# Optimization experiments

Hardware: AMD Instinct MI355X
Metric: run time of the kernel (lower is better)

## Reference

```python
import jax, jax.numpy as jnp
import numpy as np

GRID_SPACING = 0.5  # tf.constant(0.5)


def _mlp(x, W1, b1, W2, b2, W3, b3):
    # tiny base_model: 3 -> H -> H -> 1, positive output (softplus head)
    h = jnp.tanh(x @ W1 + b1)
    h = jnp.tanh(h @ W2 + b2)
    return jax.nn.softplus(h @ W3 + b3)


def setup_inputs() -> dict:
    key = jax.random.key(0)
    ks = jax.random.split(key, 8)
    nx = ny = nz = 128
    N = nx * ny * nz
    Ns = (nx - 1) * (ny - 1) * (nz - 1)
    B, H = 32768, 128
    DATAX = jax.random.uniform(ks[0], (N, 3), dtype=jnp.float32)
    DATAF = jax.random.uniform(ks[1], (N, 1), dtype=jnp.float32)
    STAGX = jax.random.uniform(ks[2], (Ns, 3), dtype=jnp.float32)
    LAPLF = jax.random.uniform(ks[3], (nx - 2, ny - 2, nz - 2), dtype=jnp.float32)
    center_indices = jax.random.randint(ks[4], (B,), 0, N, dtype=jnp.int32)
    W1 = jax.random.normal(ks[5], (3, H), dtype=jnp.float32) * 0.5
    W2 = jax.random.normal(ks[6], (H, H), dtype=jnp.float32) * (1.0 / np.sqrt(H))
    W3 = jax.random.normal(ks[7], (H, 1), dtype=jnp.float32) * (1.0 / np.sqrt(H))
    return {
        'DATAX': DATAX, 'DATAF': DATAF, 'STAGX': STAGX, 'LAPLF': LAPLF,
        'loss_m_weight': jnp.full((1,), 0.5, dtype=jnp.float32),
        'W1': W1, 'b1': jnp.zeros((H,), jnp.float32),
        'W2': W2, 'b2': jnp.zeros((H,), jnp.float32),
        'W3': W3, 'b3': jnp.zeros((1,), jnp.float32),
        'center_indices': center_indices,
    }


def reference(DATAX, DATAF, STAGX, LAPLF, loss_m_weight,
              W1, b1, W2, b2, W3, b3, center_indices):
    nxm2, nym2, nzm2 = LAPLF.shape
    nx, ny, nz = nxm2 + 2, nym2 + 2, nzm2 + 2
    N = nx * ny * nz
    Ns = (nx - 1) * (ny - 1) * (nz - 1)
    ci = center_indices.astype(jnp.int32)

    # decode flat id (z-major: z*nx*ny + y*nx + x)
    i_z = ci // (nx * ny)
    rem = ci % (nx * ny)
    i_y = rem // nx
    i_x = rem % nx
    valid = ((i_x >= 1) & (i_x < nx - 1) & (i_y >= 1) & (i_y < ny - 1)
             & (i_z >= 1) & (i_z < nz - 1))

    # 8 original-grid corners: dx,dy,dz in {-1,1}, dz fastest (list-comp order)
    off = jnp.array([-1, 1], jnp.int32)
    dd = jnp.stack(jnp.meshgrid(off, off, off, indexing='ij'), -1).reshape(8, 3)
    ox = i_x[:, None] + dd[None, :, 0]
    oy = i_y[:, None] + dd[None, :, 1]
    oz = i_z[:, None] + dd[None, :, 2]
    flat_o = jnp.clip(oz * nx * ny + oy * nx + ox, 0, N - 1)  # [B,8]

    # 8 staggered-grid corners: dx,dy,dz in {-1,0}, flat = x*ny'*nz' + y*nz' + z
    offs = jnp.array([-1, 0], jnp.int32)
    ds = jnp.stack(jnp.meshgrid(offs, offs, offs, indexing='ij'), -1).reshape(8, 3)
    sx = i_x[:, None] + ds[None, :, 0]
    sy = i_y[:, None] + ds[None, :, 1]
    sz = i_z[:, None] + ds[None, :, 2]
    flat_s = jnp.clip(sx * (ny - 1) * (nz - 1) + sy * (nz - 1) + sz, 0, Ns - 1)

    fo = _mlp(DATAX[flat_o], W1, b1, W2, b2, W3, b3)[..., 0]  # [B,8]
    fs = _mlp(STAGX[flat_s], W1, b1, W2, b2, W3, b3)[..., 0]  # [B,8]

    # diagonals of the [2,2,2] cube: (000,111),(010,101),(001,110),(011,100)
    ia = jnp.array([0, 2, 1, 3])
    ib = jnp.array([7, 5, 6, 4])
    num = jnp.abs(fo[:, ia] + fo[:, ib] - fs[:, ia] - fs[:, ib])
    den = fo[:, ia] + fo[:, ib] + fs[:, ia] + fs[:, ib]
    delta = 3.0 * (GRID_SPACING ** 2)
    lap = jnp.sum(num / den, axis=1) / (3.0 * delta)  # [B]

    flat_l = jnp.clip((i_x - 1) * nym2 * nzm2 + (i_y - 1) * nzm2 + (i_z - 1),
                      0, nxm2 * nym2 * nzm2 - 1)
    dlap = LAPLF.reshape(-1)[flat_l] - lap
    m = valid.astype(dlap.dtype)
    loss_m = loss_m_weight[0] * (jnp.sum(jnp.square(dlap) * m)
                                 / jnp.maximum(jnp.sum(m), 1.0))

    pred = _mlp(DATAX[ci], W1, b1, W2, b2, W3, b3)[:, 0]
    loss_e = jnp.mean(jnp.abs(pred - DATAF[ci][:, 0]))
    return loss_e + loss_m
```

## Files before the change

### kernel.cpp

```cpp
#include <hip/hip_runtime.h>
#include <stdint.h>

#define NXC   128
#define NXY   16384
#define NTOT  2097152
#define NS    2048383
#define SXY   16129
#define SYC   127
#define LXY   15876
#define LTOT  2000376

#define SCALE 2.8853900817779268f

typedef __bf16 bf16x8 __attribute__((ext_vector_type(8)));
typedef float f32x4 __attribute__((ext_vector_type(4)));
typedef float f32x2 __attribute__((ext_vector_type(2)));

typedef const __attribute__((address_space(1))) uint32_t* gas_t;
typedef __attribute__((address_space(3))) uint32_t* las_t;

__device__ __forceinline__ float rcp_hw(float x) {
#if __has_builtin(__builtin_amdgcn_rcpf)
  return __builtin_amdgcn_rcpf(x);
#else
  return 1.0f / x;
#endif
}
__device__ __forceinline__ float exp2_hw(float x) {
#if __has_builtin(__builtin_amdgcn_exp2f)
  return __builtin_amdgcn_exp2f(x);
#else
  return __exp2f(x);
#endif
}

__device__ __forceinline__ f32x2 tanh_pre2(f32x2 z) {
  f32x2 e;
  e.x = exp2_hw(z.x);
  e.y = exp2_hw(z.y);
  f32x2 ep1 = e + 1.0f;
  f32x2 r;
  r.x = rcp_hw(ep1.x);
  r.y = rcp_hw(ep1.y);
  return 1.0f - 2.0f * r;
}
__device__ __forceinline__ float tanh_pre(float z) {
  float e = exp2_hw(z);
  return fmaf(-2.0f, rcp_hw(e + 1.0f), 1.0f);
}

__device__ __forceinline__ float softplus_f(float x) {
  float a = fabsf(x);
  return fmaxf(x, 0.0f) + __logf(1.0f + __expf(-a));
}

__device__ __forceinline__ void ld8v(const float* p, f32x2* o) {
  float4 a = *reinterpret_cast<const float4*>(p);
  float4 b = *reinterpret_cast<const float4*>(p + 4);
  o[0].x = a.x; o[0].y = a.y;
  o[1].x = a.z; o[1].y = a.w;
  o[2].x = b.x; o[2].y = b.y;
  o[3].x = b.z; o[3].y = b.w;
}

__global__ __launch_bounds__(256) void conv_kernel(
    const float* __restrict__ W1, const float* __restrict__ B1,
    const float* __restrict__ W2, const float* __restrict__ B2,
    const float* __restrict__ W3,
    __bf16* __restrict__ w2pre, float* __restrict__ smallpre)
{
  const int n = blockIdx.x * 256 + threadIdx.x;
  if (n < 2048) {
    const int c = n >> 7, j = n & 127;
    bf16x8 v;
    #pragma unroll
    for (int e = 0; e < 8; ++e) v[e] = (__bf16)(SCALE * W2[(8 * c + e) * 128 + j]);
    *reinterpret_cast<bf16x8*>(&w2pre[(j << 7) + (((c ^ (j & 15)) & 15) << 3)]) = v;
  }
  if (blockIdx.x == 0) {
    for (int i = threadIdx.x; i < 768; i += 256) {
      float v;
      if (i < 384)      v = SCALE * W1[i];
      else if (i < 512) v = SCALE * B1[i - 384];
      else if (i < 640) v = SCALE * B2[i - 512];
      else              v = W3[i - 640];
      smallpre[i] = v;
    }
  }
}

__global__ __launch_bounds__(512) void mlp_kernel(
    const float* __restrict__ DATAX, const float* __restrict__ STAGX,
    const int* __restrict__ CI,
    const __bf16* __restrict__ w2pre, const float* __restrict__ smallpre,
    const float* __restrict__ B3, float* __restrict__ fout)
{
  __shared__ __align__(16) __bf16 w2t[16384];
  __shared__ __align__(16) float smallb[768];

  const int tid  = threadIdx.x;
  const int lane = tid & 63;
  const int wid  = tid >> 6;
  const int cl   = lane & 15;
  const int g    = lane >> 4;

  const int group = (blockIdx.x << 3) + wid;
  const int gbase = group << 6;
  const int p = gbase + lane;
  const unsigned bb = (unsigned)p / 17u;
  const int t = p - (int)bb * 17;
  const int ci = CI[bb];

  {
    const char* gsrc = (const char*)w2pre + (wid << 12) + (lane << 4);
    char*       ldst = (char*)w2t + (wid << 12);
    #pragma unroll
    for (int i = 0; i < 4; ++i) {
      __builtin_amdgcn_global_load_lds(
          (gas_t)(const void*)(gsrc + (i << 10)),
          (las_t)(void*)(ldst + (i << 10)), 16, 0, 0);
    }
    if (wid == 7) {
      const char* gs = (const char*)smallpre + (lane << 4);
      char*       ld = (char*)smallb;
      #pragma unroll
      for (int i = 0; i < 3; ++i) {
        __builtin_amdgcn_global_load_lds(
            (gas_t)(const void*)(gs + (i << 10)),
            (las_t)(void*)(ld + (i << 10)), 16, 0, 0);
      }
    }
  }

  const int iz = ci >> 14, rem = ci & 16383, iy = rem >> 7, ix = rem & 127;
  const float* xp;
  if (t < 8) {
    int ox = ix + ((t & 4) ? 1 : -1);
    int oy = iy + ((t & 2) ? 1 : -1);
    int oz = iz + ((t & 1) ? 1 : -1);
    int fl = oz * NXY + oy * NXC + ox;
    fl = min(max(fl, 0), NTOT - 1);
    xp = DATAX + 3 * fl;
  } else if (t < 16) {
    int ts = t - 8;
    int sx = ix + ((ts & 4) ? 0 : -1);
    int sy = iy + ((ts & 2) ? 0 : -1);
    int sz = iz + ((ts & 1) ? 0 : -1);
    int fl = sx * SXY + sy * SYC + sz;
    fl = min(max(fl, 0), NS - 1);
    xp = STAGX + 3 * fl;
  } else {
    xp = DATAX + 3 * ci;
  }
  const float px = xp[0], py = xp[1], pz = xp[2];
  const float b3v = B3[0];

  __syncthreads();

  const float* w1s = smallb;
  const float* b1s = smallb + 384;
  const float* b2s = smallb + 512;
  const float* w3s = smallb + 640;

  float rxv[4], ryv[4], rzv[4];
  #pragma unroll
  for (int mt = 0; mt < 4; ++mt) {
    int src = (mt << 4) + cl;
    rxv[mt] = __shfl(px, src);
    ryv[mt] = __shfl(py, src);
    rzv[mt] = __shfl(pz, src);
  }

  bf16x8 A[4][4];
  #pragma unroll
  for (int kt = 0; kt < 4; ++kt) {
    int k0 = (kt << 5) + (g << 3);
    f32x2 wx2[4], wy2[4], wz2[4], bv2[4];
    ld8v(&w1s[k0], wx2);
    ld8v(&w1s[128 + k0], wy2);
    ld8v(&w1s[256 + k0], wz2);
    ld8v(&b1s[k0], bv2);
    #pragma unroll
    for (int mt = 0; mt < 4; ++mt) {
      #pragma unroll
      for (int i = 0; i < 4; ++i) {
        f32x2 pre = rxv[mt] * wx2[i] + ryv[mt] * wy2[i]
                  + rzv[mt] * wz2[i] + bv2[i];
        f32x2 th = tanh_pre2(pre);
        A[mt][kt][2 * i]     = (__bf16)th.x;
        A[mt][kt][2 * i + 1] = (__bf16)th.y;
      }
    }
  }

  f32x2 s2[4][2];
  #pragma unroll
  for (int mt = 0; mt < 4; ++mt) {
    s2[mt][0] = 0.0f;
    s2[mt][1] = 0.0f;
  }

  #pragma unroll
  for (int nt = 0; nt < 8; ++nt) {
    const float b2v = b2s[cl + (nt << 4)];
    const float w3v = w3s[cl + (nt << 4)];
    f32x4 cc[4];
    #pragma unroll
    for (int mt = 0; mt < 4; ++mt) {
      f32x4 seed = {b2v, b2v, b2v, b2v};
      cc[mt] = seed;
    }
    const int row = (nt << 4) + cl;
    #pragma unroll
    for (int kt = 0; kt < 4; ++kt) {
      int chunk = (kt << 2) + g;
      bf16x8 bfv = *reinterpret_cast<const bf16x8*>(
          &w2t[(row << 7) + ((chunk ^ cl) << 3)]);
      #pragma unroll
      for (int mt = 0; mt < 4; ++mt)
        cc[mt] = __builtin_amdgcn_mfma_f32_16x16x32_bf16(A[mt][kt], bfv, cc[mt], 0, 0, 0);
    }
    #pragma unroll
    for (int mt = 0; mt < 4; ++mt) {
      f32x2 lo, hi;
      lo.x = cc[mt][0]; lo.y = cc[mt][1];
      hi.x = cc[mt][2]; hi.y = cc[mt][3];
      s2[mt][0] += tanh_pre2(lo) * w3v;
      s2[mt][1] += tanh_pre2(hi) * w3v;
    }
  }

  float s[4][4];
  #pragma unroll
  for (int mt = 0; mt < 4; ++mt) {
    s[mt][0] = s2[mt][0].x; s[mt][1] = s2[mt][0].y;
    s[mt][2] = s2[mt][1].x; s[mt][3] = s2[mt][1].y;
    #pragma unroll
    for (int r = 0; r < 4; ++r) {
      float v = s[mt][r];
      v += __shfl_xor(v, 1);
      v += __shfl_xor(v, 2);
      v += __shfl_xor(v, 4);
      v += __shfl_xor(v, 8);
      s[mt][r] = v;
    }
  }
  if (cl == 0) {
    #pragma unroll
    for (int mt = 0; mt < 4; ++mt) {
      int base = gbase + (mt << 4) + (g << 2);
      float4 o;
      o.x = softplus_f(s[mt][0] + b3v);
      o.y = softplus_f(s[mt][1] + b3v);
      o.z = softplus_f(s[mt][2] + b3v);
      o.w = softplus_f(s[mt][3] + b3v);
      *reinterpret_cast<float4*>(&fout[base]) = o;
    }
  }
}

__global__ __launch_bounds__(256) void reduce1(
    const float* __restrict__ f, const int* __restrict__ CI,
    const float* __restrict__ LAPLF, const float* __restrict__ DATAF,
    float* __restrict__ partials, int B)
{
  const int tid = threadIdx.x;
  const int b = blockIdx.x * 256 + tid;
  float sq = 0.f, mv = 0.f, ae = 0.f;
  if (b < B) {
    int ci = CI[b];
    int iz = ci >> 14, rem = ci & 16383, iy = rem >> 7, ix = rem & 127;
    bool valid = (ix >= 1) & (ix < 127) & (iy >= 1) & (iy < 127) &
                 (iz >= 1) & (iz < 127);
    const float* fb = f + b * 17;
    float fo[8], fs[8];
    #pragma unroll
    for (int i = 0; i < 8; ++i) { fo[i] = fb[i]; fs[i] = fb[8 + i]; }
    float pred = fb[16];
    const int ia[4] = {0, 2, 1, 3};
    const int ib[4] = {7, 5, 6, 4};
    float lap = 0.f;
    #pragma unroll
    for (int r = 0; r < 4; ++r) {
      float aa = fo[ia[r]] + fo[ib[r]];
      float bs = fs[ia[r]] + fs[ib[r]];
      lap += fabsf(aa - bs) / (aa + bs);
    }
    lap *= (1.0f / 2.25f);
    int fl = (ix - 1) * LXY + (iy - 1) * 126 + (iz - 1);
    fl = min(max(fl, 0), LTOT - 1);
    float dlap = LAPLF[fl] - lap;
    if (valid) { sq = dlap * dlap; mv = 1.f; }
    ae = fabsf(pred - DATAF[ci]);
  }
  #pragma unroll
  for (int msk = 32; msk >= 1; msk >>= 1) {
    sq += __shfl_xor(sq, msk);
    mv += __shfl_xor(mv, msk);
    ae += __shfl_xor(ae, msk);
  }
  __shared__ float rs[3][4];
  int lane = tid & 63, wd = tid >> 6;
  if (lane == 0) { rs[0][wd] = sq; rs[1][wd] = mv; rs[2][wd] = ae; }
  __syncthreads();
  if (tid == 0) {
    partials[blockIdx.x * 3 + 0] = rs[0][0] + rs[0][1] + rs[0][2] + rs[0][3];
    partials[blockIdx.x * 3 + 1] = rs[1][0] + rs[1][1] + rs[1][2] + rs[1][3];
    partials[blockIdx.x * 3 + 2] = rs[2][0] + rs[2][1] + rs[2][2] + rs[2][3];
  }
}

__global__ __launch_bounds__(128) void reduce2(
    const float* __restrict__ partials, const float* __restrict__ lw,
    float* __restrict__ out, int np, float invB)
{
  const int t = threadIdx.x;
  float sq = 0.f, mv = 0.f, ae = 0.f;
  for (int i = t; i < np; i += 128) {
    sq += partials[3 * i + 0];
    mv += partials[3 * i + 1];
    ae += partials[3 * i + 2];
  }
  #pragma unroll
  for (int msk = 32; msk >= 1; msk >>= 1) {
    sq += __shfl_xor(sq, msk);
    mv += __shfl_xor(mv, msk);
    ae += __shfl_xor(ae, msk);
  }
  __shared__ float rs[3][2];
  int lane = t & 63, wd = t >> 6;
  if (lane == 0) { rs[0][wd] = sq; rs[1][wd] = mv; rs[2][wd] = ae; }
  __syncthreads();
  if (t == 0) {
    float S = rs[0][0] + rs[0][1];
    float M = rs[1][0] + rs[1][1];
    float A = rs[2][0] + rs[2][1];
    out[0] = lw[0] * (S / fmaxf(M, 1.0f)) + A * invB;
  }
}

extern "C" void kernel_launch(void* const* d_in, const int* in_sizes, int n_in,
                              void* d_out, int out_size, void* d_ws, size_t ws_size,
                              hipStream_t stream) {
  const float* DATAX = (const float*)d_in[0];
  const float* DATAF = (const float*)d_in[1];
  const float* STAGX = (const float*)d_in[2];
  const float* LAPLF = (const float*)d_in[3];
  const float* LW    = (const float*)d_in[4];
  const float* W1    = (const float*)d_in[5];
  const float* B1    = (const float*)d_in[6];
  const float* W2    = (const float*)d_in[7];
  const float* B2    = (const float*)d_in[8];
  const float* W3    = (const float*)d_in[9];
  const float* B3    = (const float*)d_in[10];
  const int*   CI    = (const int*)d_in[11];

  const int B = in_sizes[11];
  const int P = 17 * B;
  const int ngroups = P >> 6;
  const int nblocks = ngroups >> 3;

  __bf16* w2pre    = (__bf16*)d_ws;
  float*  smallpre = (float*)((char*)d_ws + 32768);
  float*  fbuf     = (float*)((char*)d_ws + 36864);
  float*  partials = fbuf + P;

  conv_kernel<<<8, 256, 0, stream>>>(W1, B1, W2, B2, W3, w2pre, smallpre);
  mlp_kernel<<<nblocks, 512, 0, stream>>>(DATAX, STAGX, CI, w2pre, smallpre,
                                          B3, fbuf);
  const int nb2 = (B + 255) >> 8;
  reduce1<<<nb2, 256, 0, stream>>>(fbuf, CI, LAPLF, DATAF, partials, B);
  reduce2<<<1, 128, 0, stream>>>(partials, LW, (float*)d_out, nb2, 1.0f / (float)B);
}
```

Measured before the change: 66.49 us.

## Halve MLP block size and read small weights straight from global memory

The MLP kernel now runs 256-thread blocks with four waves each, so there are twice as many blocks and each wave copies 8 KB of the W2 tile into LDS. The small W1/B1/B2/W3 vectors are no longer staged in shared memory; they are read directly from global (cached) memory. B2 and W3 are interleaved so one float2 load fetches both. Smaller blocks may raise occupancy and scheduling flexibility, at the cost of copying W2 into LDS twice as often in total and serving the small-weight reads from cache instead of LDS.

```diff
diff --git a/kernel.cpp b/kernel.cpp
--- a/kernel.cpp
+++ b/kernel.cpp
@@ -43,10 +43,6 @@
   r.x = rcp_hw(ep1.x);
   r.y = rcp_hw(ep1.y);
   return 1.0f - 2.0f * r;
-}
-__device__ __forceinline__ float tanh_pre(float z) {
-  float e = exp2_hw(z);
-  return fmaf(-2.0f, rcp_hw(e + 1.0f), 1.0f);
 }
 
 __device__ __forceinline__ float softplus_f(float x) {
@@ -82,21 +78,22 @@
       float v;
       if (i < 384)      v = SCALE * W1[i];
       else if (i < 512) v = SCALE * B1[i - 384];
-      else if (i < 640) v = SCALE * B2[i - 512];
-      else              v = W3[i - 640];
+      else {
+        int q = (i - 512) >> 1;
+        v = ((i & 1) == 0) ? (SCALE * B2[q]) : W3[q];
+      }
       smallpre[i] = v;
     }
   }
 }
 
-__global__ __launch_bounds__(512) void mlp_kernel(
+__global__ __launch_bounds__(256) void mlp_kernel(
     const float* __restrict__ DATAX, const float* __restrict__ STAGX,
     const int* __restrict__ CI,
     const __bf16* __restrict__ w2pre, const float* __restrict__ smallpre,
     const float* __restrict__ B3, float* __restrict__ fout)
 {
   __shared__ __align__(16) __bf16 w2t[16384];
-  __shared__ __align__(16) float smallb[768];
 
   const int tid  = threadIdx.x;
   const int lane = tid & 63;
@@ -104,7 +101,7 @@
   const int cl   = lane & 15;
   const int g    = lane >> 4;
 
-  const int group = (blockIdx.x << 3) + wid;
+  const int group = (blockIdx.x << 2) + wid;
   const int gbase = group << 6;
   const int p = gbase + lane;
   const unsigned bb = (unsigned)p / 17u;
@@ -112,23 +109,13 @@
   const int ci = CI[bb];
 
   {
-    const char* gsrc = (const char*)w2pre + (wid << 12) + (lane << 4);
-    char*       ldst = (char*)w2t + (wid << 12);
-    #pragma unroll
-    for (int i = 0; i < 4; ++i) {
+    const char* gsrc = (const char*)w2pre + (wid << 13) + (lane << 4);
+    char*       ldst = (char*)w2t + (wid << 13);
+    #pragma unroll
+    for (int i = 0; i < 8; ++i) {
       __builtin_amdgcn_global_load_lds(
           (gas_t)(const void*)(gsrc + (i << 10)),
           (las_t)(void*)(ldst + (i << 10)), 16, 0, 0);
-    }
-    if (wid == 7) {
-      const char* gs = (const char*)smallpre + (lane << 4);
-      char*       ld = (char*)smallb;
-      #pragma unroll
-      for (int i = 0; i < 3; ++i) {
-        __builtin_amdgcn_global_load_lds(
-            (gas_t)(const void*)(gs + (i << 10)),
-            (las_t)(void*)(ld + (i << 10)), 16, 0, 0);
-      }
     }
   }
 
@@ -155,12 +142,11 @@
   const float px = xp[0], py = xp[1], pz = xp[2];
   const float b3v = B3[0];
 
+  const float* w1s = smallpre;
+  const float* b1s = smallpre + 384;
+  const float* bw  = smallpre + 512;
+
   __syncthreads();
-
-  const float* w1s = smallb;
-  const float* b1s = smallb + 384;
-  const float* b2s = smallb + 512;
-  const float* w3s = smallb + 640;
 
   float rxv[4], ryv[4], rzv[4];
   #pragma unroll
@@ -202,8 +188,8 @@
 
   #pragma unroll
   for (int nt = 0; nt < 8; ++nt) {
-    const float b2v = b2s[cl + (nt << 4)];
-    const float w3v = w3s[cl + (nt << 4)];
+    const float2 bwv = *reinterpret_cast<const float2*>(&bw[(cl + (nt << 4)) << 1]);
+    const float b2v = bwv.x, w3v = bwv.y;
     f32x4 cc[4];
     #pragma unroll
     for (int mt = 0; mt < 4; ++mt) {
@@ -358,7 +344,7 @@
   const int B = in_sizes[11];
   const int P = 17 * B;
   const int ngroups = P >> 6;
-  const int nblocks = ngroups >> 3;
+  const int nblocks = ngroups >> 2;
 
   __bf16* w2pre    = (__bf16*)d_ws;
   float*  smallpre = (float*)((char*)d_ws + 32768);
@@ -366,7 +352,7 @@
   float*  partials = fbuf + P;
 
   conv_kernel<<<8, 256, 0, stream>>>(W1, B1, W2, B2, W3, w2pre, smallpre);
-  mlp_kernel<<<nblocks, 512, 0, stream>>>(DATAX, STAGX, CI, w2pre, smallpre,
+  mlp_kernel<<<nblocks, 256, 0, stream>>>(DATAX, STAGX, CI, w2pre, smallpre,
                                           B3, fbuf);
   const int nb2 = (B + 255) >> 8;
   reduce1<<<nb2, 256, 0, stream>>>(fbuf, CI, LAPLF, DATAF, partials, B);
```

Result: faster. 64.52 us, median of 2 (-3.0%).
